# Kernel optimization log

Measured on AMD Instinct MI355X. Metric: run time of the kernel, lower is better.

The kernel has to match this reference:

```python
import jax, jax.numpy as jnp
import numpy as np

B, S, E, H, D, W = 2, 4096, 768, 12, 64, 256  # batch, seq, hidden, heads, head_dim, one-sided window


def setup_inputs() -> dict:
    key = jax.random.key(0)
    ks = jax.random.split(key, 4)
    s = 0.02
    return {
        "hidden_states": jax.random.normal(ks[0], (B, S, E), jnp.float32),
        "Wq": jax.random.normal(ks[1], (E, E), jnp.float32) * s,
        "bq": jnp.zeros((E,), jnp.float32),
        "Wk": jax.random.normal(ks[2], (E, E), jnp.float32) * s,
        "bk": jnp.zeros((E,), jnp.float32),
        "Wv": jax.random.normal(ks[3], (E, E), jnp.float32) * s,
        "bv": jnp.zeros((E,), jnp.float32),
    }


def _band_attention(q, k, v):
    # q,k,v: [B,H,S,D]. Sliding-window attention: query i attends keys j with |j-i| <= W,
    # clipped to [0, S) -- same math as sliding_chunks_matmul_qk + mask_invalid_locations
    # + softmax + sliding_chunks_matmul_pv (dropout p=0, eval mode).
    C = S // W  # number of query chunks of size W

    def ext(x):
        # gather, for each chunk c, the keys of chunks c-1, c, c+1 (zero padded at edges)
        xp = jnp.pad(x, ((0, 0), (0, 0), (W, W), (0, 0)))
        xc = xp.reshape(B, H, C + 2, W, D)
        return jnp.concatenate([xc[:, :, 0:C], xc[:, :, 1:C + 1], xc[:, :, 2:C + 2]], axis=3)  # [B,H,C,3W,D]

    qc = q.reshape(B, H, C, W, D)
    ke = ext(k)
    ve = ext(v)
    scores = jnp.einsum('bhcpd,bhctd->bhcpt', qc, ke)  # [B,H,C,W,3W]

    p = jnp.arange(W)[:, None]            # query offset within chunk
    t = jnp.arange(3 * W)[None, :]        # key offset within extended window
    rel = t - W - p                       # j - i  (relative position)
    j = jnp.arange(C)[:, None, None] * W + (t - W)[None]  # global key index [C,W,3W]
    mask = (jnp.abs(rel)[None] <= W) & (j >= 0) & (j < S)  # band + sequence-boundary mask

    scores = jnp.where(mask[None, None], scores, -1e30)
    probs = jax.nn.softmax(scores, axis=-1)
    out = jnp.einsum('bhcpt,bhctd->bhcpd', probs, ve)
    return out.reshape(B, H, S, D)


def reference(hidden_states, Wq, bq, Wk, bk, Wv, bv):
    scale = 1.0 / float(np.sqrt(D))
    q = (hidden_states @ Wq + bq) * scale  # q scaled by 1/sqrt(head_dim) as in original
    k = hidden_states @ Wk + bk
    v = hidden_states @ Wv + bv
    split = lambda x: x.reshape(B, S, H, D).transpose(0, 2, 1, 3)  # [B,H,S,D]
    out = _band_attention(split(q), split(k), split(v))
    return out.transpose(0, 2, 1, 3).reshape(B, S, E)  # [B,S,E] context_layer
```

## Files before the change

### kernel.cpp

```cpp
#include <hip/hip_runtime.h>

#define BB 2
#define SS 4096
#define EE 768
#define HH 12
#define DD 64
#define WW 256

typedef __attribute__((ext_vector_type(8))) short short8;
typedef __attribute__((ext_vector_type(4))) short short4v;
typedef __attribute__((ext_vector_type(4))) float floatx4;

#define MFMA16(a, b, c) __builtin_amdgcn_mfma_f32_16x16x32_bf16(a, b, c, 0, 0, 0)

__device__ __forceinline__ float bf2f(short x) {
    union { unsigned u; float f; } v;
    v.u = ((unsigned)(unsigned short)x) << 16;
    return v.f;
}

__device__ __forceinline__ short f2bf(float x) {
    union { float f; unsigned u; } v;
    v.f = x;
    unsigned r = v.u + 0x7fffu + ((v.u >> 16) & 1u);
    return (short)(r >> 16);
}

__device__ __forceinline__ int imin(int a, int b) { return a < b ? a : b; }
__device__ __forceinline__ int imax(int a, int b) { return a > b ? a : b; }

__device__ __forceinline__ void gload_lds16(const short* g, short* l) {
    __builtin_amdgcn_global_load_lds(
        (const __attribute__((address_space(1))) unsigned*)g,
        (__attribute__((address_space(3))) unsigned*)l, 16, 0, 0);
}

__global__ __launch_bounds__(256) void prep(
    const float* __restrict__ hidden, const float* __restrict__ W0,
    const float* __restrict__ W1, const float* __restrict__ W2,
    short* __restrict__ Xb, short* __restrict__ Wt) {
    __shared__ short t[32][33];
    int bid = blockIdx.x;
    if (bid < 3072) {
        int i = bid * 256 + threadIdx.x;
        const floatx4* src = (const floatx4*)(hidden + (size_t)i * 8);
        floatx4 f0 = src[0], f1 = src[1];
        short8 s8;
#pragma unroll
        for (int j = 0; j < 4; j++) { s8[j] = f2bf(f0[j]); s8[j + 4] = f2bf(f1[j]); }
        *(short8*)(Xb + (size_t)i * 8) = s8;
    } else {
        int tmp = bid - 3072;
        int z = tmp / 576, r = tmp % 576;
        int bx = r % 24, by = r / 24;
        const float* in = (z == 0) ? W0 : (z == 1) ? W1 : W2;
        short* op = Wt + (size_t)z * EE * EE;
        int tx = threadIdx.x & 31, ty = threadIdx.x >> 5;
        int x = bx * 32 + tx, y0 = by * 32;
        for (int j = 0; j < 32; j += 8) t[ty + j][tx] = f2bf(in[(size_t)(y0 + ty + j) * EE + x]);
        __syncthreads();
        int x2 = y0 + tx, y2 = bx * 32;
        for (int j = 0; j < 32; j += 8) op[(size_t)(y2 + ty + j) * EE + x2] = t[tx][ty + j];
    }
}

__global__ __launch_bounds__(256) void qkv_gemm(
    const short* __restrict__ Xb, const short* __restrict__ Wt,
    const float* __restrict__ Bq, const float* __restrict__ Bk, const float* __restrict__ Bv,
    short* __restrict__ Qo, short* __restrict__ Ko, short* __restrict__ Vto) {
    int z = blockIdx.z;
    const short* Wz = Wt + (size_t)z * EE * EE;
    const float* bias = (z == 0) ? Bq : (z == 1) ? Bk : Bv;

    __shared__ __align__(16) short As[128 * 32];
    __shared__ __align__(16) short Bs[128 * 32];
    int tid = threadIdx.x;
    int m0 = blockIdx.x * 128, n0 = blockIdx.y * 128;
    int wave = tid >> 6, lane = tid & 63, lquad = lane >> 4, lrow = lane & 15;
    int wm = (wave & 1) * 64, wn = (wave >> 1) * 64;

    floatx4 acc[4][4] = {};

    int c0 = tid, c1 = 256 + tid;
    int r0s = c0 >> 2, c0s = (c0 & 3) * 8;
    int r1s = c1 >> 2, c1s = (c1 & 3) * 8;

    for (int k0 = 0; k0 < EE; k0 += 32) {
        gload_lds16(&Xb[(size_t)(m0 + r0s) * EE + k0 + c0s], &As[c0 * 8]);
        gload_lds16(&Wz[(size_t)(n0 + r0s) * EE + k0 + c0s], &Bs[c0 * 8]);
        gload_lds16(&Xb[(size_t)(m0 + r1s) * EE + k0 + c1s], &As[c1 * 8]);
        gload_lds16(&Wz[(size_t)(n0 + r1s) * EE + k0 + c1s], &Bs[c1 * 8]);
        __syncthreads();
        short8 af[4], bfv[4];
#pragma unroll
        for (int mt = 0; mt < 4; mt++)
            af[mt] = *(short8*)&As[(wm + mt * 16 + lrow) * 32 + lquad * 8];
#pragma unroll
        for (int nt = 0; nt < 4; nt++)
            bfv[nt] = *(short8*)&Bs[(wn + nt * 16 + lrow) * 32 + lquad * 8];
#pragma unroll
        for (int mt = 0; mt < 4; mt++)
#pragma unroll
            for (int nt = 0; nt < 4; nt++)
                acc[mt][nt] = MFMA16(af[mt], bfv[nt], acc[mt][nt]);
        __syncthreads();
    }

    if (z == 2) {
        for (int nt = 0; nt < 4; nt++) {
            int gn = n0 + wn + nt * 16 + lrow;
            float bv = bias[gn];
            int h = gn >> 6, d = gn & 63;
            for (int mt = 0; mt < 4; mt++) {
                int gm0 = m0 + wm + mt * 16 + lquad * 4;
                int b = gm0 >> 12, s = gm0 & (SS - 1);
                short4v pk;
                for (int r = 0; r < 4; r++) pk[r] = f2bf(acc[mt][nt][r] + bv);
                *(short4v*)&Vto[(((size_t)(b * HH + h)) * DD + d) * SS + s] = pk;
            }
        }
    } else {
        short* out = (z == 0) ? Qo : Ko;
        float scale = (z == 0) ? 0.125f : 1.0f;
        for (int nt = 0; nt < 4; nt++) {
            int gn = n0 + wn + nt * 16 + lrow;
            float bv = bias[gn];
            int h = gn >> 6, d = gn & 63;
            for (int mt = 0; mt < 4; mt++) {
                int gmb = m0 + wm + mt * 16 + lquad * 4;
                for (int r = 0; r < 4; r++) {
                    int gm = gmb + r;
                    int b = gm >> 12, s = gm & (SS - 1);
                    float v = (acc[mt][nt][r] + bv) * scale;
                    out[(((size_t)(b * HH + h)) * SS + s) * DD + d] = f2bf(v);
                }
            }
        }
    }
}

__global__ __launch_bounds__(256) void band_attn(
    const short* __restrict__ Q, const short* __restrict__ K,
    const short* __restrict__ Vt, float* __restrict__ out) {
    int hb = blockIdx.x;
    int h = hb % HH, b = hb / HH;
    int chunk = blockIdx.y;
    int tid = threadIdx.x;
    int wave = tid >> 6, lane = tid & 63, lquad = lane >> 4, lrow = lane & 15;
    int qbase = chunk * 128 + wave * 32;

    const short* Qh = Q + ((size_t)(b * HH + h)) * SS * DD;
    const short* Kh = K + ((size_t)(b * HH + h)) * SS * DD;
    const short* Vh = Vt + ((size_t)(b * HH + h)) * DD * SS;

    __shared__ __align__(16) short Ks[2][64 * 72];
    __shared__ __align__(16) short Vs[2][64 * 72];
    __shared__ __align__(16) short Ps[4][16 * 72];
    short* Pw = &Ps[wave][0];

    short8 qf[2][2];
#pragma unroll
    for (int m = 0; m < 2; m++)
#pragma unroll
        for (int hh = 0; hh < 2; hh++)
            qf[m][hh] = *(const short8*)&Qh[(size_t)(qbase + m * 16 + lrow) * DD + hh * 32 + lquad * 8];

    floatx4 o[2][4] = {};
    float ls[2] = {0.0f, 0.0f};

    int kwin = chunk * 128 - WW;
    int srow = tid >> 3;
    int scol = (tid & 7) * 8;
    int tlo = wave >> 1;

    short8 kreg[2], vreg[2];
    auto loadTile = [&](int t) {
        int ks0 = kwin + t * 64;
#pragma unroll
        for (int i = 0; i < 2; i++) {
            int r = srow + i * 32;
            int gk = imin(imax(ks0 + r, 0), SS - 1);
            kreg[i] = *(const short8*)&Kh[(size_t)gk * DD + scol];
            int gv = imin(imax(ks0 + scol, 0), SS - 8);
            vreg[i] = *(const short8*)&Vh[(size_t)r * SS + gv];
        }
    };
    auto storeTile = [&](int buf) {
#pragma unroll
        for (int i = 0; i < 2; i++) {
            int r = srow + i * 32;
            *(short8*)&Ks[buf][r * 72 + scol] = kreg[i];
            *(short8*)&Vs[buf][r * 72 + scol] = vreg[i];
        }
    };

    loadTile(0);
    storeTile(0);
    __syncthreads();

    for (int t = 0; t < 10; t++) {
        int buf = t & 1;
        if (t < 9) loadTile(t + 1);

        if ((unsigned)(t - tlo) < 9u) {
            int ks0 = kwin + t * 64;
            short8 kf[4][2], vf[4][2];
#pragma unroll
            for (int kt = 0; kt < 4; kt++)
#pragma unroll
                for (int hh = 0; hh < 2; hh++)
                    kf[kt][hh] = *(short8*)&Ks[buf][(kt * 16 + lrow) * 72 + hh * 32 + lquad * 8];
#pragma unroll
            for (int nt = 0; nt < 4; nt++)
#pragma unroll
                for (int hh = 0; hh < 2; hh++)
                    vf[nt][hh] = *(short8*)&Vs[buf][(nt * 16 + lrow) * 72 + hh * 32 + lquad * 8];

            int d0 = ks0 - qbase;
            bool interior = (d0 >= -225) && (d0 <= 193) && (ks0 >= 0) && (ks0 <= SS - 64);

#pragma unroll
            for (int m = 0; m < 2; m++) {
                int q = qbase + m * 16 + lrow;
                floatx4 s[4];
#pragma unroll
                for (int kt = 0; kt < 4; kt++) {
                    floatx4 zz = {};
                    s[kt] = MFMA16(kf[kt][0], qf[m][0], zz);
                    s[kt] = MFMA16(kf[kt][1], qf[m][1], s[kt]);
                }
                float lacc = 0.0f;
                if (interior) {
#pragma unroll
                    for (int kt = 0; kt < 4; kt++) {
                        short4v pk;
#pragma unroll
                        for (int r = 0; r < 4; r++) {
                            float p = __expf(s[kt][r]);
                            pk[r] = f2bf(p);
                            lacc += bf2f(pk[r]);
                        }
                        *(short4v*)&Pw[lrow * 72 + kt * 16 + lquad * 4] = pk;
                    }
                } else {
#pragma unroll
                    for (int kt = 0; kt < 4; kt++) {
                        short4v pk;
#pragma unroll
                        for (int r = 0; r < 4; r++) {
                            int key = ks0 + kt * 16 + lquad * 4 + r;
                            bool valid = ((unsigned)(key - q + WW) <= 2u * WW) && ((unsigned)key < SS);
                            float p = valid ? __expf(s[kt][r]) : 0.0f;
                            pk[r] = f2bf(p);
                            lacc += bf2f(pk[r]);
                        }
                        *(short4v*)&Pw[lrow * 72 + kt * 16 + lquad * 4] = pk;
                    }
                }
                ls[m] += lacc;
                asm volatile("" ::: "memory");
                short8 ap0 = *(short8*)&Pw[lrow * 72 + lquad * 8];
                short8 ap1 = *(short8*)&Pw[lrow * 72 + 32 + lquad * 8];
#pragma unroll
                for (int nt = 0; nt < 4; nt++) {
                    o[m][nt] = MFMA16(ap0, vf[nt][0], o[m][nt]);
                    o[m][nt] = MFMA16(ap1, vf[nt][1], o[m][nt]);
                }
            }
        }

        if (t < 9) storeTile(buf ^ 1);
        __syncthreads();
    }

#pragma unroll
    for (int m = 0; m < 2; m++) {
        ls[m] += __shfl_xor(ls[m], 16, 64);
        ls[m] += __shfl_xor(ls[m], 32, 64);
        ls[m] = 1.0f / ls[m];
    }

#pragma unroll
    for (int m = 0; m < 2; m++) {
#pragma unroll
        for (int r = 0; r < 4; r++) {
            float linv = __shfl(ls[m], lquad * 4 + r, 64);
            int s = qbase + m * 16 + lquad * 4 + r;
#pragma unroll
            for (int nt = 0; nt < 4; nt++)
                out[((size_t)b * SS + s) * EE + h * DD + nt * 16 + lrow] = o[m][nt][r] * linv;
        }
    }
}

extern "C" void kernel_launch(void* const* d_in, const int* in_sizes, int n_in,
                              void* d_out, int out_size, void* d_ws, size_t ws_size,
                              hipStream_t stream) {
    const float* hidden = (const float*)d_in[0];
    const float* Wq = (const float*)d_in[1];
    const float* bq = (const float*)d_in[2];
    const float* Wk = (const float*)d_in[3];
    const float* bk = (const float*)d_in[4];
    const float* Wv = (const float*)d_in[5];
    const float* bv = (const float*)d_in[6];
    float* out = (float*)d_out;

    short* ws = (short*)d_ws;
    const size_t WSZ = (size_t)EE * EE;
    const size_t QSZ = (size_t)BB * HH * SS * DD;
    short* Wt = ws;
    short* Qb = Wt + 3 * WSZ;
    short* Kb = Qb + QSZ;
    short* Vtb = Kb + QSZ;
    short* Xb = (short*)d_out;

    prep<<<dim3(3072 + 3 * 576, 1, 1), 256, 0, stream>>>(hidden, Wq, Wk, Wv, Xb, Wt);

    qkv_gemm<<<dim3(64, 6, 3), 256, 0, stream>>>(Xb, Wt, bq, bk, bv, Qb, Kb, Vtb);

    band_attn<<<dim3(HH * BB, SS / 128, 1), 256, 0, stream>>>(Qb, Kb, Vtb, out);
}
```

Measured before the change: 181.9 us.

## Triple-buffer LDS tiles in QKV GEMM with async prefetch two steps ahead

The QKV projection GEMM moves from a single LDS buffer with two barriers per k-step to a three-stage ring of LDS buffers. Tiles are prefetched two iterations ahead with direct global-to-LDS loads, and an explicit vmcnt wait plus one barrier per step replaces the second __syncthreads. The aim is to overlap global memory latency with MFMA work. In exchange the GEMM uses three times the LDS, which may lower occupancy, and correctness now depends on hand-written waitcnt counts.

```diff
diff --git a/kernel.cpp b/kernel.cpp
--- a/kernel.cpp
+++ b/kernel.cpp
@@ -72,8 +72,8 @@
     const short* Wz = Wt + (size_t)z * EE * EE;
     const float* bias = (z == 0) ? Bq : (z == 1) ? Bk : Bv;
 
-    __shared__ __align__(16) short As[128 * 32];
-    __shared__ __align__(16) short Bs[128 * 32];
+    __shared__ __align__(16) short As[3][128 * 32];
+    __shared__ __align__(16) short Bs[3][128 * 32];
     int tid = threadIdx.x;
     int m0 = blockIdx.x * 128, n0 = blockIdx.y * 128;
     int wave = tid >> 6, lane = tid & 63, lquad = lane >> 4, lrow = lane & 15;
@@ -85,25 +85,46 @@
     int r0s = c0 >> 2, c0s = (c0 & 3) * 8;
     int r1s = c1 >> 2, c1s = (c1 & 3) * 8;
 
-    for (int k0 = 0; k0 < EE; k0 += 32) {
-        gload_lds16(&Xb[(size_t)(m0 + r0s) * EE + k0 + c0s], &As[c0 * 8]);
-        gload_lds16(&Wz[(size_t)(n0 + r0s) * EE + k0 + c0s], &Bs[c0 * 8]);
-        gload_lds16(&Xb[(size_t)(m0 + r1s) * EE + k0 + c1s], &As[c1 * 8]);
-        gload_lds16(&Wz[(size_t)(n0 + r1s) * EE + k0 + c1s], &Bs[c1 * 8]);
-        __syncthreads();
+    const short* xa0 = &Xb[(size_t)(m0 + r0s) * EE + c0s];
+    const short* wa0 = &Wz[(size_t)(n0 + r0s) * EE + c0s];
+    const short* xa1 = &Xb[(size_t)(m0 + r1s) * EE + c1s];
+    const short* wa1 = &Wz[(size_t)(n0 + r1s) * EE + c1s];
+
+    auto issueTile = [&](int t) {
+        int k0 = t * 32;
+        int bs = t % 3;
+        gload_lds16(xa0 + k0, &As[bs][c0 * 8]);
+        gload_lds16(wa0 + k0, &Bs[bs][c0 * 8]);
+        gload_lds16(xa1 + k0, &As[bs][c1 * 8]);
+        gload_lds16(wa1 + k0, &Bs[bs][c1 * 8]);
+    };
+
+    issueTile(0);
+    issueTile(1);
+
+#pragma unroll
+    for (int t = 0; t < 24; ++t) {
+        if (t < 23) asm volatile("s_waitcnt vmcnt(4)" ::: "memory");
+        else        asm volatile("s_waitcnt vmcnt(0)" ::: "memory");
+        __builtin_amdgcn_sched_barrier(0);
+        __builtin_amdgcn_s_barrier();
+        asm volatile("" ::: "memory");
+
+        if (t + 2 < 24) issueTile(t + 2);
+
+        int bs = t % 3;
         short8 af[4], bfv[4];
 #pragma unroll
         for (int mt = 0; mt < 4; mt++)
-            af[mt] = *(short8*)&As[(wm + mt * 16 + lrow) * 32 + lquad * 8];
+            af[mt] = *(short8*)&As[bs][(wm + mt * 16 + lrow) * 32 + lquad * 8];
 #pragma unroll
         for (int nt = 0; nt < 4; nt++)
-            bfv[nt] = *(short8*)&Bs[(wn + nt * 16 + lrow) * 32 + lquad * 8];
+            bfv[nt] = *(short8*)&Bs[bs][(wn + nt * 16 + lrow) * 32 + lquad * 8];
 #pragma unroll
         for (int mt = 0; mt < 4; mt++)
 #pragma unroll
             for (int nt = 0; nt < 4; nt++)
                 acc[mt][nt] = MFMA16(af[mt], bfv[nt], acc[mt][nt]);
-        __syncthreads();
     }
 
     if (z == 2) {
```

Measured after the change: 182.9 us. About the same (+0.6%).
